# Kernel optimization log

Hardware: AMD Instinct MI355X
Metric: run time of the kernel (lower is better)

## Reference

```python
import jax, jax.numpy as jnp
import numpy as np

B, F, H, LAT = 4, 64, 128, 512
N_CALLS = 16          # n_calls=2, module multiplies by 8
NEG = 0.2             # leaky-relu slope
EPS = 1e-5            # InstanceNorm2d eps

# hypernetwork output layout: w_in[F,3F], b_in[F], w_mid[F,F], b_mid[F], w_out[F,F], b_out[F], w_short[F,3F], b_short[F]
_sizes = [3*F*F, F, F*F, F, F*F, F, 3*F*F, F]
_off = np.cumsum([0] + _sizes)
HYP_OUT = int(_off[-1])


def _sobel_kernel():
    # SinSobel: smoothing (cos) x derivative (sin) separable 5x5 gradient filters
    lin = np.linspace(-1.0, 1.0, 5)
    d = np.sin(lin * np.pi / 2.0)
    s = np.cos(lin * np.pi / 2.0)
    gx = np.outer(s, d)                      # d/dx
    gy = np.outer(d, s)                      # d/dy
    k = np.stack([gx, gy])[:, None]          # [2,1,5,5]
    return jnp.asarray(np.tile(k, (F, 1, 1, 1)), jnp.float32)  # [2F,1,5,5] depthwise


def _conv(x, w, pad, groups=1):
    return jax.lax.conv_general_dilated(
        x, w, (1, 1), [(pad, pad), (pad, pad)],
        dimension_numbers=('NCHW', 'OIHW', 'NCHW'),
        feature_group_count=groups)


def _lrelu(x):
    return jnp.where(x >= 0, x, NEG * x)


def setup_inputs() -> dict:
    key = jax.random.key(0)
    ks = jax.random.split(key, 8)
    f32 = jnp.float32
    return {
        "lat": jax.random.normal(ks[0], (B, LAT), f32),
        "ca_init": jax.random.normal(ks[1], (B, F, H, H), f32),
        "leak_factor": jnp.asarray(0.1, f32),
        "hyper_w": jax.random.normal(ks[2], (HYP_OUT, LAT), f32) * 0.02,
        "hyper_b": jnp.zeros((HYP_OUT,), f32),
        "res_w1": jax.random.normal(ks[3], (F, F, 3, 3), f32) * 0.05,
        "res_b1": jnp.zeros((F,), f32),
        "res_w2": jax.random.normal(ks[4], (F, F, 3, 3), f32) * 0.05,
        "res_b2": jnp.zeros((F,), f32),
        "img_w": jax.random.normal(ks[5], (3, F, 3, 3), f32) * 0.05,
        "img_b": jnp.zeros((3,), f32),
    }


def reference(lat, ca_init, leak_factor, hyper_w, hyper_b,
              res_w1, res_b1, res_w2, res_b2, img_w, img_b):
    sob = _sobel_kernel()
    lf = jnp.clip(leak_factor, 0.001, 1000.0)

    # per-sample dynamic 1x1-conv weights from hypernetwork (lat is loop-invariant)
    ws = lat @ hyper_w.T + hyper_b           # [B, HYP_OUT]

    def seg(i, shape):
        return ws[:, _off[i]:_off[i + 1]].reshape((B,) + shape)
    w_in,  b_in  = seg(0, (F, 3 * F)), seg(1, (F,))
    w_mid, b_mid = seg(2, (F, F)),     seg(3, (F,))
    w_out, b_out = seg(4, (F, F)),     seg(5, (F,))
    w_sh,  b_sh  = seg(6, (F, 3 * F)), seg(7, (F,))

    def step(out, _):
        # SinSobel: identity channels + depthwise 5x5 gradients -> [B,3F,H,H]
        y = jnp.concatenate([out, _conv(out, sob, 2, groups=F)], axis=1)
        # InstanceNorm2d (affine=False)
        mu = y.mean((2, 3), keepdims=True)
        var = y.var((2, 3), keepdims=True)
        y = (y - mu) * jax.lax.rsqrt(var + EPS)
        # DynaResidualBlock: per-sample 1x1 convs (batched GEMMs) + shortcut
        h = _lrelu(jnp.einsum('bchw,boc->bohw', y, w_in) + b_in[:, :, None, None])
        h = _lrelu(jnp.einsum('bchw,boc->bohw', h, w_mid) + b_mid[:, :, None, None])
        h = jnp.einsum('bchw,boc->bohw', h, w_out) + b_out[:, :, None, None]
        sc = jnp.einsum('bchw,boc->bohw', y, w_sh) + b_sh[:, :, None, None]
        return out + lf * (h + sc), None

    out, _ = jax.lax.scan(step, ca_init, None, length=N_CALLS)

    # conv_img: ResidualBlock(3x3) then final 3x3 conv to image channels, clamp
    h = _lrelu(_conv(out, res_w1, 1) + res_b1[None, :, None, None])
    h = _conv(h, res_w2, 1) + res_b2[None, :, None, None]
    out = out + h
    img = _conv(out, img_w, 1) + img_b[None, :, None, None]
    return jnp.clip(img, -1.0, 1.0)
```

## Files before the change

### kernel.cpp

```cpp
#include <hip/hip_runtime.h>
#include <cstddef>

#define R_ 0.70710678118654752f
#define NEG_ 0.2f
#define EPS_ 1e-5f

constexpr int F_ = 64, C3_ = 192, HH_ = 128, NPIX_ = 16384, B_ = 4, LAT_ = 512, HYP_ = 33024;
constexpr int OFFI_WIN = 0, OFFI_BIN = 12288, OFFI_WMID = 12352, OFFI_BMID = 16448,
              OFFI_WOUT = 16512, OFFI_BOUT = 20608, OFFI_WSH = 20672, OFFI_BSH = 32960;
constexpr size_t OFF_HYP = 0;
constexpr size_t OFF_SRAW = 134144;
constexpr size_t OFF_WFIN = 140288;
constexpr size_t OFF_WFSH = 189440;
constexpr size_t OFF_WFMID = 238592;
constexpr size_t OFF_WFOUT = 254976;
constexpr size_t OFF_CW1 = 271360;
constexpr size_t OFF_CW2 = 308224;
constexpr size_t OFF_CWIMG = 345088;
constexpr size_t OFF_OUT = 346816;
constexpr size_t OFF_SOB = 4541120;
constexpr size_t OFF_TMP = OFF_SOB;

typedef short bf16x8 __attribute__((ext_vector_type(8)));
typedef float f32x4 __attribute__((ext_vector_type(4)));

static __device__ __forceinline__ unsigned short f2b(float v) {
  unsigned u = __builtin_bit_cast(unsigned, v);
  u += 0x7fffu + ((u >> 16) & 1u);
  return (unsigned short)(u >> 16);
}
static __device__ __forceinline__ float b2f(unsigned short h) {
  return __builtin_bit_cast(float, ((unsigned)h) << 16);
}
static __device__ __forceinline__ void split2(float v, unsigned short& hi, unsigned short& lo) {
  hi = f2b(v);
  lo = f2b(v - b2f(hi));
}

#define MM3(acc, ahi, alo, whi, wlo)                                        \
  acc = __builtin_amdgcn_mfma_f32_16x16x32_bf16(ahi, whi, acc, 0, 0, 0);    \
  acc = __builtin_amdgcn_mfma_f32_16x16x32_bf16(ahi, wlo, acc, 0, 0, 0);    \
  acc = __builtin_amdgcn_mfma_f32_16x16x32_bf16(alo, whi, acc, 0, 0, 0);

__global__ __launch_bounds__(256) void hyper_gemm_kernel(
    const float* __restrict__ lat, const float* __restrict__ hw,
    const float* __restrict__ hb, float* __restrict__ hyp) {
  __shared__ float slat[B_ * LAT_];
  const int tid = threadIdx.x;
  for (int i = tid; i < B_ * LAT_; i += 256) slat[i] = lat[i];
  __syncthreads();
  const int wave = tid >> 6, lane = tid & 63;
  const int j = blockIdx.x * 4 + wave;
  if (j >= HYP_) return;
  const float* wr = hw + (size_t)j * LAT_;
  float a0 = 0.f, a1 = 0.f, a2 = 0.f, a3 = 0.f;
  for (int i = 0; i < LAT_; i += 64) {
    float w = wr[i + lane];
    a0 = __builtin_fmaf(w, slat[0 * LAT_ + i + lane], a0);
    a1 = __builtin_fmaf(w, slat[1 * LAT_ + i + lane], a1);
    a2 = __builtin_fmaf(w, slat[2 * LAT_ + i + lane], a2);
    a3 = __builtin_fmaf(w, slat[3 * LAT_ + i + lane], a3);
  }
  #pragma unroll
  for (int off = 32; off; off >>= 1) {
    a0 += __shfl_down(a0, off, 64);
    a1 += __shfl_down(a1, off, 64);
    a2 += __shfl_down(a2, off, 64);
    a3 += __shfl_down(a3, off, 64);
  }
  if (lane == 0) {
    float b = hb[j];
    hyp[0 * HYP_ + j] = a0 + b;
    hyp[1 * HYP_ + j] = a1 + b;
    hyp[2 * HYP_ + j] = a2 + b;
    hyp[3 * HYP_ + j] = a3 + b;
  }
}

__global__ __launch_bounds__(256) void prep_dynw_kernel(float* wsm) {
  const int b = blockIdx.x >> 3, sl = blockIdx.x & 7;
  const int tid = threadIdx.x;
  const float* hyp = wsm + OFF_HYP + (size_t)b * HYP_;
  unsigned short* wfin = (unsigned short*)(wsm + OFF_WFIN) + (size_t)b * 24576;
  unsigned short* wfsh = (unsigned short*)(wsm + OFF_WFSH) + (size_t)b * 24576;
  unsigned short* wfmid = (unsigned short*)(wsm + OFF_WFMID) + (size_t)b * 8192;
  unsigned short* wfout = (unsigned short*)(wsm + OFF_WFOUT) + (size_t)b * 8192;

  if (sl < 6) {
    const int base = sl * 2048;
    for (int i = tid; i < 2048; i += 256) {
      int idx = base + i;
      int j = idx & 7, ch = (idx >> 3) & 63, g2 = (idx >> 9) & 3, ks = idx >> 11;
      int k = ks * 32 + g2 * 8 + j;
      int fbx = ((ks * 4 + g2) * 64 + ch) * 16;
      unsigned short h, l;
      split2(hyp[OFFI_WIN + ch * C3_ + k], h, l);
      wfin[fbx + j] = h; wfin[fbx + 8 + j] = l;
      split2(hyp[OFFI_WSH + ch * C3_ + k], h, l);
      wfsh[fbx + j] = h; wfsh[fbx + 8 + j] = l;
    }
  } else if (sl == 6) {
    for (int idx = tid; idx < 4096; idx += 256) {
      int j = idx & 7, ch = (idx >> 3) & 63, g2 = (idx >> 9) & 3, ks = idx >> 11;
      int k = ks * 32 + g2 * 8 + j;
      int fbx = ((ks * 4 + g2) * 64 + ch) * 16;
      unsigned short h, l;
      split2(hyp[OFFI_WMID + ch * 64 + k], h, l);
      wfmid[fbx + j] = h; wfmid[fbx + 8 + j] = l;
      split2(hyp[OFFI_WOUT + ch * 64 + k], h, l);
      wfout[fbx + j] = h; wfout[fbx + 8 + j] = l;
    }
  }
}

__global__ __launch_bounds__(256) void prep_convw_kernel(
    const float* __restrict__ w1, const float* __restrict__ w2,
    const float* __restrict__ wi, unsigned short* __restrict__ wf1,
    unsigned short* __restrict__ wf2, float* __restrict__ wit) {
  const int idx = blockIdx.x * 256 + threadIdx.x;
  if (idx < 36864) {
    int j = idx & 7, ch = (idx >> 3) & 63, fg = idx >> 9;
    int k = (fg >> 2) * 32 + (fg & 3) * 8 + j;
    int c = k & 63, t = k >> 6;
    int fb = (fg * 64 + ch) * 16;
    unsigned short h, l;
    split2(w1[(ch * 64 + c) * 9 + t], h, l);
    wf1[fb + j] = h; wf1[fb + 8 + j] = l;
    split2(w2[(ch * 64 + c) * 9 + t], h, l);
    wf2[fb + j] = h; wf2[fb + 8 + j] = l;
  }
  if (idx < 64 * 9 * 3) {
    int k = idx % 3, rest = idx / 3;
    int t = rest % 9, c = rest / 9;
    wit[idx] = wi[(k * 64 + c) * 9 + t];
  }
}

__device__ __forceinline__ void hline_z(const float* __restrict__ P, int rr, int col,
                                        float& hdv, float& hsv, float& cv) {
  if (rr < 0 || rr > 127) { hdv = 0.f; hsv = 0.f; cv = 0.f; return; }
  const float* rp = P + rr * HH_;
  float vm2 = (col >= 2) ? rp[col - 2] : 0.f;
  float vm1 = (col >= 1) ? rp[col - 1] : 0.f;
  float v0 = rp[col];
  float vp1 = (col <= 126) ? rp[col + 1] : 0.f;
  float vp2 = (col <= 125) ? rp[col + 2] : 0.f;
  hdv = -vm2 - R_ * vm1 + R_ * vp1 + vp2;
  hsv = R_ * vm1 + v0 + R_ * vp1;
  cv = v0;
}

__device__ __forceinline__ float blockReduceSum8(float v, float* scratch) {
  const int tid = threadIdx.x;
  #pragma unroll
  for (int off = 32; off; off >>= 1) v += __shfl_down(v, off, 64);
  if ((tid & 63) == 0) scratch[tid >> 6] = v;
  __syncthreads();
  float r = 0.f;
  #pragma unroll
  for (int w = 0; w < 8; ++w) r += scratch[w];
  __syncthreads();
  return r;
}

__global__ __launch_bounds__(512) void sobel_stats_kernel(
    const float* __restrict__ outb, unsigned int* __restrict__ sob,
    float* __restrict__ sraw) {
  __shared__ float scr[8];
  const int bi = blockIdx.x;
  const int q = bi & 3, c = (bi >> 2) & 63, b = bi >> 8;
  const int tid = threadIdx.x;
  const int col = tid & 127;
  const int r0 = q * 32 + (tid >> 7) * 8;
  const float* P = outb + ((size_t)(b * F_ + c)) * NPIX_;
  unsigned int* ygx = sob + ((size_t)(b * 128 + 2 * c)) * NPIX_;
  unsigned int* ygy = ygx + NPIX_;

  float sI = 0.f, qI = 0.f, sX = 0.f, qX = 0.f, sY = 0.f, qY = 0.f;
  float hd_m1, hd_0, hd_p1, hs_m2, hs_m1, hs_0, hs_p1;
  float td, tc;
  hline_z(P, r0 - 2, col, td, hs_m2, tc);
  hline_z(P, r0 - 1, col, hd_m1, hs_m1, tc);
  hline_z(P, r0, col, hd_0, hs_0, tc);
  sI += tc; qI += tc * tc;
  hline_z(P, r0 + 1, col, hd_p1, hs_p1, tc);
  sI += tc; qI += tc * tc;

  for (int i = 0; i < 8; ++i) {
    const int r = r0 + i;
    const int nr = r + 2;
    float hd_new, hs_new, cnew;
    hline_z(P, nr, col, hd_new, hs_new, cnew);
    if (nr <= r0 + 7) { sI += cnew; qI += cnew * cnew; }
    float gxv = R_ * (hd_m1 + hd_p1) + hd_0;
    float gyv = -hs_m2 - R_ * hs_m1 + R_ * hs_p1 + hs_new;
    const int o = r * HH_ + col;
    unsigned short h, l;
    split2(gxv, h, l);
    ygx[o] = ((unsigned)h << 16) | l;
    split2(gyv, h, l);
    ygy[o] = ((unsigned)h << 16) | l;
    sX += gxv; qX += gxv * gxv;
    sY += gyv; qY += gyv * gyv;
    hd_m1 = hd_0; hd_0 = hd_p1; hd_p1 = hd_new;
    hs_m2 = hs_m1; hs_m1 = hs_0; hs_0 = hs_p1; hs_p1 = hs_new;
  }
  __syncthreads();
  float tI = blockReduceSum8(sI, scr);
  float tQI = blockReduceSum8(qI, scr);
  float tX = blockReduceSum8(sX, scr);
  float tQX = blockReduceSum8(qX, scr);
  float tY = blockReduceSum8(sY, scr);
  float tQY = blockReduceSum8(qY, scr);
  if (tid == 0) {
    float* r = sraw + (size_t)bi * 6;
    r[0] = tI; r[1] = tQI; r[2] = tX; r[3] = tQX; r[4] = tY; r[5] = tQY;
  }
}

__global__ __launch_bounds__(256, 2) void mlp_mfma_kernel(
    float* __restrict__ outb, const unsigned int* __restrict__ sobu,
    const float* __restrict__ wsf, const float* __restrict__ leak) {
  __shared__ unsigned short yhi[64 * 200];
  __shared__ unsigned short ylo[64 * 200];
  __shared__ unsigned short hhi[64 * 72];
  __shared__ unsigned short hlo[64 * 72];
  __shared__ unsigned short resb[64 * 66];
  __shared__ float stl[C3_ * 2];
  __shared__ float ssig[64];
  const int bi = blockIdx.x;
  const int b = bi >> 8, t = bi & 255;
  const int px0 = t * 64;
  const int tid = threadIdx.x;

  if (tid < 64) {
    const int c = tid;
    const float* r = wsf + OFF_SRAW + ((size_t)(b * 64 + c) * 4) * 6;
    float sI = 0.f, qI = 0.f, sX = 0.f, qX = 0.f, sY = 0.f, qY = 0.f;
    #pragma unroll
    for (int q = 0; q < 4; ++q) {
      sI += r[q * 6 + 0]; qI += r[q * 6 + 1];
      sX += r[q * 6 + 2]; qX += r[q * 6 + 3];
      sY += r[q * 6 + 4]; qY += r[q * 6 + 5];
    }
    const float n = 1.f / 16384.f;
    float m, rs;
    m = sI * n; rs = rsqrtf(qI * n - m * m + EPS_);
    stl[c * 2] = m; stl[c * 2 + 1] = rs; ssig[c] = 1.f / rs;
    const int cx = 64 + 2 * c, cy = cx + 1;
    m = sX * n; stl[cx * 2] = m;          stl[cx * 2 + 1] = rsqrtf(qX * n - m * m + EPS_);
    m = sY * n; stl[cy * 2] = m;          stl[cy * 2 + 1] = rsqrtf(qY * n - m * m + EPS_);
  }
  __syncthreads();

  const float* ob = outb + (size_t)b * F_ * NPIX_;
  const unsigned int* sbp = sobu + (size_t)b * 128 * NPIX_;
  #pragma unroll
  for (int it = 0; it < 12; ++it) {
    int ci = it * 256 + tid;
    int k = ci >> 4, pq = ci & 15;
    int kk = k ^ ((pq >> 1) << 3);
    unsigned short* ph = &yhi[(pq * 4) * 200 + kk];
    unsigned short* pl = &ylo[(pq * 4) * 200 + kk];
    const float mu = stl[k * 2], inv = stl[k * 2 + 1];
    float vv[4];
    if (k < 64) {
      float4 f = *(const float4*)(ob + (size_t)k * NPIX_ + px0 + pq * 4);
      vv[0] = f.x; vv[1] = f.y; vv[2] = f.z; vv[3] = f.w;
      const float sg = ssig[k];
      #pragma unroll
      for (int e = 0; e < 4; ++e) {
        unsigned short h, l;
        split2((vv[e] - mu) * inv, h, l);
        ph[e * 200] = h; pl[e * 200] = l;
        float rec = __builtin_fmaf(b2f(h) + b2f(l), sg, mu);
        resb[k * 66 + pq * 4 + e] = f2b(vv[e] - rec);
      }
    } else {
      uint4 v = *(const uint4*)(sbp + (size_t)(k - 64) * NPIX_ + px0 + pq * 4);
      vv[0] = b2f((unsigned short)(v.x >> 16)) + b2f((unsigned short)(v.x & 0xffff));
      vv[1] = b2f((unsigned short)(v.y >> 16)) + b2f((unsigned short)(v.y & 0xffff));
      vv[2] = b2f((unsigned short)(v.z >> 16)) + b2f((unsigned short)(v.z & 0xffff));
      vv[3] = b2f((unsigned short)(v.w >> 16)) + b2f((unsigned short)(v.w & 0xffff));
      #pragma unroll
      for (int e = 0; e < 4; ++e) {
        unsigned short h, l;
        split2((vv[e] - mu) * inv, h, l);
        ph[e * 200] = h; pl[e * 200] = l;
      }
    }
  }
  __syncthreads();

  const int wave = tid >> 6, lane = tid & 63;
  const int lrow = lane & 15, g = lane >> 4;
  const int chm = wave * 16 + lrow;
  const float lf = fminf(fmaxf(leak[0], 0.001f), 1000.f);
  const float* hyp = wsf + OFF_HYP + (size_t)b * HYP_;
  const unsigned short* wfin = (const unsigned short*)(wsf + OFF_WFIN) + (size_t)b * 24576;
  const unsigned short* wfsh = (const unsigned short*)(wsf + OFF_WFSH) + (size_t)b * 24576;
  const unsigned short* wfmid = (const unsigned short*)(wsf + OFF_WFMID) + (size_t)b * 8192;
  const unsigned short* wfout = (const unsigned short*)(wsf + OFF_WFOUT) + (size_t)b * 8192;

  f32x4 aH[4], aS[4];
  {
    float b1 = hyp[OFFI_BIN + chm], b2 = hyp[OFFI_BSH + chm];
    #pragma unroll
    for (int pf = 0; pf < 4; ++pf) {
      aH[pf] = (f32x4){b1, b1, b1, b1};
      aS[pf] = (f32x4){b2, b2, b2, b2};
    }
  }
  #pragma unroll
  for (int ks = 0; ks < 6; ++ks) {
    const size_t wo = (size_t)((ks * 4 + g) * 64 + chm) * 16;
    bf16x8 whiI = *(const bf16x8*)(wfin + wo);
    bf16x8 wloI = *(const bf16x8*)(wfin + wo + 8);
    bf16x8 whiS = *(const bf16x8*)(wfsh + wo);
    bf16x8 wloS = *(const bf16x8*)(wfsh + wo + 8);
    #pragma unroll
    for (int pf = 0; pf < 4; ++pf) {
      const int pxl = pf * 16 + lrow;
      const int kb = pxl * 200 + ((ks * 32 + g * 8) ^ ((pxl >> 3) << 3));
      bf16x8 ahi = *(const bf16x8*)&yhi[kb];
      bf16x8 alo = *(const bf16x8*)&ylo[kb];
      MM3(aH[pf], ahi, alo, whiI, wloI);
      MM3(aS[pf], ahi, alo, whiS, wloS);
    }
  }
  #pragma unroll
  for (int pf = 0; pf < 4; ++pf) {
    #pragma unroll
    for (int j = 0; j < 4; ++j) {
      float v = aH[pf][j];
      v = (v >= 0.f) ? v : NEG_ * v;
      unsigned short h, l;
      split2(v, h, l);
      const int o = (pf * 16 + g * 4 + j) * 72 + chm;
      hhi[o] = h; hlo[o] = l;
    }
  }
  __syncthreads();
  f32x4 aM[4];
  {
    float bm = hyp[OFFI_BMID + chm];
    #pragma unroll
    for (int pf = 0; pf < 4; ++pf) aM[pf] = (f32x4){bm, bm, bm, bm};
  }
  #pragma unroll
  for (int ks = 0; ks < 2; ++ks) {
    const size_t wo = (size_t)((ks * 4 + g) * 64 + chm) * 16;
    bf16x8 whi = *(const bf16x8*)(wfmid + wo);
    bf16x8 wlo = *(const bf16x8*)(wfmid + wo + 8);
    #pragma unroll
    for (int pf = 0; pf < 4; ++pf) {
      const int kb = (pf * 16 + lrow) * 72 + ks * 32 + g * 8;
      bf16x8 ahi = *(const bf16x8*)&hhi[kb];
      bf16x8 alo = *(const bf16x8*)&hlo[kb];
      MM3(aM[pf], ahi, alo, whi, wlo);
    }
  }
  __syncthreads();
  #pragma unroll
  for (int pf = 0; pf < 4; ++pf) {
    #pragma unroll
    for (int j = 0; j < 4; ++j) {
      float v = aM[pf][j];
      v = (v >= 0.f) ? v : NEG_ * v;
      unsigned short h, l;
      split2(v, h, l);
      const int o = (pf * 16 + g * 4 + j) * 72 + chm;
      hhi[o] = h; hlo[o] = l;
    }
  }
  __syncthreads();
  f32x4 aO[4];
  {
    float bo = hyp[OFFI_BOUT + chm];
    #pragma unroll
    for (int pf = 0; pf < 4; ++pf) aO[pf] = (f32x4){bo, bo, bo, bo};
  }
  #pragma unroll
  for (int ks = 0; ks < 2; ++ks) {
    const size_t wo = (size_t)((ks * 4 + g) * 64 + chm) * 16;
    bf16x8 whi = *(const bf16x8*)(wfout + wo);
    bf16x8 wlo = *(const bf16x8*)(wfout + wo + 8);
    #pragma unroll
    for (int pf = 0; pf < 4; ++pf) {
      const int kb = (pf * 16 + lrow) * 72 + ks * 32 + g * 8;
      bf16x8 ahi = *(const bf16x8*)&hhi[kb];
      bf16x8 alo = *(const bf16x8*)&hlo[kb];
      MM3(aO[pf], ahi, alo, whi, wlo);
    }
  }
  const float mu_c = stl[chm * 2];
  const float sg_c = ssig[chm];
  #pragma unroll
  for (int pf = 0; pf < 4; ++pf) {
    float* op = outb + ((size_t)(b * F_ + chm)) * NPIX_ + px0 + pf * 16 + g * 4;
    f32x4 nv;
    #pragma unroll
    for (int j = 0; j < 4; ++j) {
      const int pxl = pf * 16 + g * 4 + j;
      const int kk2 = chm ^ ((pxl >> 3) << 3);
      float yv = b2f(yhi[pxl * 200 + kk2]) + b2f(ylo[pxl * 200 + kk2]);
      float vorig = __builtin_fmaf(yv, sg_c, mu_c) + b2f(resb[chm * 66 + pxl]);
      nv[j] = vorig + lf * (aO[pf][j] + aS[pf][j]);
    }
    *(f32x4*)op = nv;
  }
}

__global__ __launch_bounds__(256, 2) void conv_mfma_kernel(
    const float* __restrict__ in, const unsigned short* __restrict__ wf,
    const float* __restrict__ bias, float* __restrict__ dst, int mode) {
  __shared__ unsigned short ahi[4 * 72 * 64];
  __shared__ unsigned short alo[4 * 72 * 64];
  const int bi = blockIdx.x;
  const int b = bi >> 7, rest = bi & 127;
  const int row0 = (rest >> 1) * 2, colbase = (rest & 1) << 6;
  const int tid = threadIdx.x;
  const float* ip = in + (size_t)b * F_ * NPIX_;

  for (int idx = tid; idx < 4608; idx += 256) {
    const int chunk = idx % 18;
    const int rowp = (idx / 18) % 4;
    const int ch = idx / 72;
    const int r2 = row0 - 1 + rowp;
    const int gcol0 = colbase - 4 + chunk * 4;
    float4 v;
    if (r2 < 0 || r2 > 127) {
      v = make_float4(0.f, 0.f, 0.f, 0.f);
    } else if (gcol0 >= 0 && gcol0 <= 124) {
      v = *(const float4*)(ip + (size_t)ch * NPIX_ + r2 * HH_ + gcol0);
    } else {
      const float* rp = ip + (size_t)ch * NPIX_ + r2 * HH_;
      v.x = (gcol0 >= 0 && gcol0 < 128) ? rp[gcol0] : 0.f;
      v.y = (gcol0 + 1 >= 0 && gcol0 + 1 < 128) ? rp[gcol0 + 1] : 0.f;
      v.z = (gcol0 + 2 >= 0 && gcol0 + 2 < 128) ? rp[gcol0 + 2] : 0.f;
      v.w = (gcol0 + 3 >= 0 && gcol0 + 3 < 128) ? rp[gcol0 + 3] : 0.f;
    }
    const float vv[4] = {v.x, v.y, v.z, v.w};
    #pragma unroll
    for (int e = 0; e < 4; ++e) {
      const int i = chunk * 4 + e;
      const int sw = (((i >> 2) & 7) ^ ((i & 3) << 1) ^ rowp) << 3;
      const int a = (rowp * 72 + i) * 64 + (ch ^ sw);
      unsigned short h, l;
      split2(vv[e], h, l);
      ahi[a] = h; alo[a] = l;
    }
  }
  __syncthreads();

  const int wave = tid >> 6, lane = tid & 63;
  const int lrow = lane & 15, g = lane >> 4;
  const int pxl = wave * 16 + lrow;
  f32x4 acc0[4], acc1[4];
  #pragma unroll
  for (int cg = 0; cg < 4; ++cg) {
    float bz = bias[cg * 16 + lrow];
    acc0[cg] = (f32x4){bz, bz, bz, bz};
    acc1[cg] = (f32x4){bz, bz, bz, bz};
  }
  for (int ks = 0; ks < 18; ++ks) {
    const int kbase = ks * 32 + g * 8;
    const int t = kbase >> 6, c0 = kbase & 63;
    const int dy = t / 3 - 1, dx = t % 3 - 1;
    const int i = pxl + 4 + dx;
    const int rp0 = 1 + dy, rp1 = 2 + dy;
    const int sw0 = (((i >> 2) & 7) ^ ((i & 3) << 1) ^ rp0) << 3;
    const int sw1 = (((i >> 2) & 7) ^ ((i & 3) << 1) ^ rp1) << 3;
    const int a0 = (rp0 * 72 + i) * 64 + (c0 ^ sw0);
    const int a1 = (rp1 * 72 + i) * 64 + (c0 ^ sw1);
    bf16x8 ah0 = *(const bf16x8*)&ahi[a0];
    bf16x8 al0 = *(const bf16x8*)&alo[a0];
    bf16x8 ah1 = *(const bf16x8*)&ahi[a1];
    bf16x8 al1 = *(const bf16x8*)&alo[a1];
    #pragma unroll
    for (int cg = 0; cg < 4; ++cg) {
      const unsigned short* wp = wf + (size_t)((ks * 4 + g) * 64 + cg * 16 + lrow) * 16;
      bf16x8 whi = *(const bf16x8*)wp;
      bf16x8 wlo = *(const bf16x8*)(wp + 8);
      MM3(acc0[cg], ah0, al0, whi, wlo);
      MM3(acc1[cg], ah1, al1, whi, wlo);
    }
  }
  #pragma unroll
  for (int r = 0; r < 2; ++r) {
    #pragma unroll
    for (int cg = 0; cg < 4; ++cg) {
      const f32x4 av = r ? acc1[cg] : acc0[cg];
      float* op = dst + ((size_t)(b * F_ + cg * 16 + lrow)) * NPIX_ + (row0 + r) * HH_ +
                  colbase + wave * 16 + g * 4;
      if (mode == 1) {
        f32x4 rr;
        #pragma unroll
        for (int j = 0; j < 4; ++j) {
          float v = av[j];
          rr[j] = (v >= 0.f) ? v : NEG_ * v;
        }
        *(f32x4*)op = rr;
      } else {
        f32x4 cur = *(f32x4*)op;
        #pragma unroll
        for (int j = 0; j < 4; ++j) cur[j] += av[j];
        *(f32x4*)op = cur;
      }
    }
  }
}

__global__ __launch_bounds__(256, 4) void convimg_kernel(
    const float* __restrict__ outb, const float* __restrict__ wT,
    const float* __restrict__ bias, float* __restrict__ img) {
  __shared__ float part[2 * 128 * 3];
  const int bi = blockIdx.x;
  const int b = bi >> 7, pxb = bi & 127;
  const int tid = threadIdx.x;
  const int px = tid & 127;
  const int hf = __builtin_amdgcn_readfirstlane(tid >> 7);
  const int p = pxb * 128 + px;
  const int row = p >> 7, col = p & 127;
  float a0 = 0.f, a1 = 0.f, a2 = 0.f;
  const float* ip = outb + (size_t)b * F_ * NPIX_;
  for (int cc = 0; cc < 32; ++cc) {
    const int c = hf * 32 + cc;
    const float* pl = ip + (size_t)c * NPIX_;
    #pragma unroll
    for (int t = 0; t < 9; ++t) {
      const int dy = t / 3 - 1, dx = t % 3 - 1;
      const int r2 = row + dy, c2 = col + dx;
      float v = (r2 >= 0 && r2 < 128 && c2 >= 0 && c2 < 128) ? pl[r2 * HH_ + c2] : 0.f;
      const float* wp = wT + (c * 9 + t) * 3;
      a0 = __builtin_fmaf(v, wp[0], a0);
      a1 = __builtin_fmaf(v, wp[1], a1);
      a2 = __builtin_fmaf(v, wp[2], a2);
    }
  }
  part[(hf * 128 + px) * 3 + 0] = a0;
  part[(hf * 128 + px) * 3 + 1] = a1;
  part[(hf * 128 + px) * 3 + 2] = a2;
  __syncthreads();
  if (hf == 0) {
    float r0 = a0 + part[(128 + px) * 3 + 0] + bias[0];
    float r1 = a1 + part[(128 + px) * 3 + 1] + bias[1];
    float r2 = a2 + part[(128 + px) * 3 + 2] + bias[2];
    img[((size_t)b * 3 + 0) * NPIX_ + p] = fminf(fmaxf(r0, -1.f), 1.f);
    img[((size_t)b * 3 + 1) * NPIX_ + p] = fminf(fmaxf(r1, -1.f), 1.f);
    img[((size_t)b * 3 + 2) * NPIX_ + p] = fminf(fmaxf(r2, -1.f), 1.f);
  }
}

extern "C" void kernel_launch(void* const* d_in, const int* in_sizes, int n_in,
                              void* d_out, int out_size, void* d_ws, size_t ws_size,
                              hipStream_t stream) {
  const float* lat = (const float*)d_in[0];
  const float* ca_init = (const float*)d_in[1];
  const float* leak = (const float*)d_in[2];
  const float* hyper_w = (const float*)d_in[3];
  const float* hyper_b = (const float*)d_in[4];
  const float* res_w1 = (const float*)d_in[5];
  const float* res_b1 = (const float*)d_in[6];
  const float* res_w2 = (const float*)d_in[7];
  const float* res_b2 = (const float*)d_in[8];
  const float* img_w = (const float*)d_in[9];
  const float* img_b = (const float*)d_in[10];
  float* out = (float*)d_out;
  float* ws = (float*)d_ws;
  unsigned int* sobu = (unsigned int*)(ws + OFF_SOB);

  hyper_gemm_kernel<<<(HYP_ + 3) / 4, 256, 0, stream>>>(lat, hyper_w, hyper_b, ws + OFF_HYP);
  prep_dynw_kernel<<<32, 256, 0, stream>>>(ws);
  prep_convw_kernel<<<144, 256, 0, stream>>>(res_w1, res_w2, img_w,
                                             (unsigned short*)(ws + OFF_CW1),
                                             (unsigned short*)(ws + OFF_CW2),
                                             ws + OFF_CWIMG);
  hipMemcpyAsync(ws + OFF_OUT, ca_init, (size_t)B_ * F_ * NPIX_ * sizeof(float),
                 hipMemcpyDeviceToDevice, stream);

  for (int st = 0; st < 16; ++st) {
    sobel_stats_kernel<<<1024, 512, 0, stream>>>(ws + OFF_OUT, sobu, ws + OFF_SRAW);
    mlp_mfma_kernel<<<1024, 256, 0, stream>>>(ws + OFF_OUT, sobu, ws, leak);
  }

  conv_mfma_kernel<<<512, 256, 0, stream>>>(ws + OFF_OUT, (const unsigned short*)(ws + OFF_CW1),
                                            res_b1, (float*)(ws + OFF_TMP), 1);
  conv_mfma_kernel<<<512, 256, 0, stream>>>((const float*)(ws + OFF_TMP),
                                            (const unsigned short*)(ws + OFF_CW2),
                                            res_b2, ws + OFF_OUT, 2);
  convimg_kernel<<<512, 256, 0, stream>>>(ws + OFF_OUT, ws + OFF_CWIMG, img_b, out);
}
```

Baseline: 879.8 us.

## Stage MLP input in two channel halves to cut LDS and raise occupancy

The MLP kernel now stages the normalized 192-channel input in two 96-channel chunks, shrinking the shared-memory buffers, and drops the residual side buffer. It re-reads the state from global memory for the final update instead of reconstructing it from LDS. Launch bounds go from 2 to 3 blocks per CU. Separately, the image conv kernel is split into 64-pixel tiles with four channel-quarter waves, doubling the grid. The cost is an extra barrier per MLP block and an additional global read of the state.

New measurement: 852.2 us (median of 2 runs). -3.1%, faster.

```diff
diff --git a/kernel.cpp b/kernel.cpp
--- a/kernel.cpp
+++ b/kernel.cpp
@@ -218,16 +218,14 @@
   }
 }
 
-__global__ __launch_bounds__(256, 2) void mlp_mfma_kernel(
+__global__ __launch_bounds__(256, 3) void mlp_mfma_kernel(
     float* __restrict__ outb, const unsigned int* __restrict__ sobu,
     const float* __restrict__ wsf, const float* __restrict__ leak) {
-  __shared__ unsigned short yhi[64 * 200];
-  __shared__ unsigned short ylo[64 * 200];
-  __shared__ unsigned short hhi[64 * 72];
-  __shared__ unsigned short hlo[64 * 72];
-  __shared__ unsigned short resb[64 * 66];
+  __shared__ unsigned short yhi[64 * 136];
+  __shared__ unsigned short ylo[64 * 136];
+  __shared__ unsigned short hhi[64 * 66];
+  __shared__ unsigned short hlo[64 * 66];
   __shared__ float stl[C3_ * 2];
-  __shared__ float ssig[64];
   const int bi = blockIdx.x;
   const int b = bi >> 8, t = bi & 255;
   const int px0 = t * 64;
@@ -244,9 +242,8 @@
       sY += r[q * 6 + 4]; qY += r[q * 6 + 5];
     }
     const float n = 1.f / 16384.f;
-    float m, rs;
-    m = sI * n; rs = rsqrtf(qI * n - m * m + EPS_);
-    stl[c * 2] = m; stl[c * 2 + 1] = rs; ssig[c] = 1.f / rs;
+    float m;
+    m = sI * n; stl[c * 2] = m;           stl[c * 2 + 1] = rsqrtf(qI * n - m * m + EPS_);
     const int cx = 64 + 2 * c, cy = cx + 1;
     m = sX * n; stl[cx * 2] = m;          stl[cx * 2 + 1] = rsqrtf(qX * n - m * m + EPS_);
     m = sY * n; stl[cy * 2] = m;          stl[cy * 2 + 1] = rsqrtf(qY * n - m * m + EPS_);
@@ -255,43 +252,6 @@
 
   const float* ob = outb + (size_t)b * F_ * NPIX_;
   const unsigned int* sbp = sobu + (size_t)b * 128 * NPIX_;
-  #pragma unroll
-  for (int it = 0; it < 12; ++it) {
-    int ci = it * 256 + tid;
-    int k = ci >> 4, pq = ci & 15;
-    int kk = k ^ ((pq >> 1) << 3);
-    unsigned short* ph = &yhi[(pq * 4) * 200 + kk];
-    unsigned short* pl = &ylo[(pq * 4) * 200 + kk];
-    const float mu = stl[k * 2], inv = stl[k * 2 + 1];
-    float vv[4];
-    if (k < 64) {
-      float4 f = *(const float4*)(ob + (size_t)k * NPIX_ + px0 + pq * 4);
-      vv[0] = f.x; vv[1] = f.y; vv[2] = f.z; vv[3] = f.w;
-      const float sg = ssig[k];
-      #pragma unroll
-      for (int e = 0; e < 4; ++e) {
-        unsigned short h, l;
-        split2((vv[e] - mu) * inv, h, l);
-        ph[e * 200] = h; pl[e * 200] = l;
-        float rec = __builtin_fmaf(b2f(h) + b2f(l), sg, mu);
-        resb[k * 66 + pq * 4 + e] = f2b(vv[e] - rec);
-      }
-    } else {
-      uint4 v = *(const uint4*)(sbp + (size_t)(k - 64) * NPIX_ + px0 + pq * 4);
-      vv[0] = b2f((unsigned short)(v.x >> 16)) + b2f((unsigned short)(v.x & 0xffff));
-      vv[1] = b2f((unsigned short)(v.y >> 16)) + b2f((unsigned short)(v.y & 0xffff));
-      vv[2] = b2f((unsigned short)(v.z >> 16)) + b2f((unsigned short)(v.z & 0xffff));
-      vv[3] = b2f((unsigned short)(v.w >> 16)) + b2f((unsigned short)(v.w & 0xffff));
-      #pragma unroll
-      for (int e = 0; e < 4; ++e) {
-        unsigned short h, l;
-        split2((vv[e] - mu) * inv, h, l);
-        ph[e * 200] = h; pl[e * 200] = l;
-      }
-    }
-  }
-  __syncthreads();
-
   const int wave = tid >> 6, lane = tid & 63;
   const int lrow = lane & 15, g = lane >> 4;
   const int chm = wave * 16 + lrow;
@@ -312,20 +272,56 @@
     }
   }
   #pragma unroll
-  for (int ks = 0; ks < 6; ++ks) {
-    const size_t wo = (size_t)((ks * 4 + g) * 64 + chm) * 16;
-    bf16x8 whiI = *(const bf16x8*)(wfin + wo);
-    bf16x8 wloI = *(const bf16x8*)(wfin + wo + 8);
-    bf16x8 whiS = *(const bf16x8*)(wfsh + wo);
-    bf16x8 wloS = *(const bf16x8*)(wfsh + wo + 8);
-    #pragma unroll
-    for (int pf = 0; pf < 4; ++pf) {
-      const int pxl = pf * 16 + lrow;
-      const int kb = pxl * 200 + ((ks * 32 + g * 8) ^ ((pxl >> 3) << 3));
-      bf16x8 ahi = *(const bf16x8*)&yhi[kb];
-      bf16x8 alo = *(const bf16x8*)&ylo[kb];
-      MM3(aH[pf], ahi, alo, whiI, wloI);
-      MM3(aS[pf], ahi, alo, whiS, wloS);
+  for (int c0 = 0; c0 < 2; ++c0) {
+    if (c0) __syncthreads();
+    #pragma unroll
+    for (int it = 0; it < 6; ++it) {
+      const int ci = it * 256 + tid;
+      const int kl = ci >> 4, pq = ci & 15;
+      const int k = c0 * 96 + kl;
+      const int kk = kl ^ ((pq >> 1) << 3);
+      unsigned short* ph = &yhi[(pq * 4) * 136 + kk];
+      unsigned short* pl = &ylo[(pq * 4) * 136 + kk];
+      const float mu = stl[k * 2], inv = stl[k * 2 + 1];
+      if (k < 64) {
+        float4 f = *(const float4*)(ob + (size_t)k * NPIX_ + px0 + pq * 4);
+        const float vv[4] = {f.x, f.y, f.z, f.w};
+        #pragma unroll
+        for (int e = 0; e < 4; ++e) {
+          unsigned short h, l;
+          split2((vv[e] - mu) * inv, h, l);
+          ph[e * 136] = h; pl[e * 136] = l;
+        }
+      } else {
+        uint4 v = *(const uint4*)(sbp + (size_t)(k - 64) * NPIX_ + px0 + pq * 4);
+        const unsigned uu[4] = {v.x, v.y, v.z, v.w};
+        #pragma unroll
+        for (int e = 0; e < 4; ++e) {
+          float val = b2f((unsigned short)(uu[e] >> 16)) + b2f((unsigned short)(uu[e] & 0xffff));
+          unsigned short h, l;
+          split2((val - mu) * inv, h, l);
+          ph[e * 136] = h; pl[e * 136] = l;
+        }
+      }
+    }
+    __syncthreads();
+    #pragma unroll
+    for (int ks3 = 0; ks3 < 3; ++ks3) {
+      const int ks = c0 * 3 + ks3;
+      const size_t wo = (size_t)((ks * 4 + g) * 64 + chm) * 16;
+      bf16x8 whiI = *(const bf16x8*)(wfin + wo);
+      bf16x8 wloI = *(const bf16x8*)(wfin + wo + 8);
+      bf16x8 whiS = *(const bf16x8*)(wfsh + wo);
+      bf16x8 wloS = *(const bf16x8*)(wfsh + wo + 8);
+      #pragma unroll
+      for (int pf = 0; pf < 4; ++pf) {
+        const int pxl = pf * 16 + lrow;
+        const int kb = pxl * 136 + ((ks3 * 32 + g * 8) ^ ((pxl >> 3) << 3));
+        bf16x8 ahi = *(const bf16x8*)&yhi[kb];
+        bf16x8 alo = *(const bf16x8*)&ylo[kb];
+        MM3(aH[pf], ahi, alo, whiI, wloI);
+        MM3(aS[pf], ahi, alo, whiS, wloS);
+      }
     }
   }
   #pragma unroll
@@ -336,7 +332,7 @@
       v = (v >= 0.f) ? v : NEG_ * v;
       unsigned short h, l;
       split2(v, h, l);
-      const int o = (pf * 16 + g * 4 + j) * 72 + chm;
+      const int o = (pf * 16 + g * 4 + j) * 66 + chm;
       hhi[o] = h; hlo[o] = l;
     }
   }
@@ -354,7 +350,7 @@
     bf16x8 wlo = *(const bf16x8*)(wfmid + wo + 8);
     #pragma unroll
     for (int pf = 0; pf < 4; ++pf) {
-      const int kb = (pf * 16 + lrow) * 72 + ks * 32 + g * 8;
+      const int kb = (pf * 16 + lrow) * 66 + ks * 32 + g * 8;
       bf16x8 ahi = *(const bf16x8*)&hhi[kb];
       bf16x8 alo = *(const bf16x8*)&hlo[kb];
       MM3(aM[pf], ahi, alo, whi, wlo);
@@ -369,7 +365,7 @@
       v = (v >= 0.f) ? v : NEG_ * v;
       unsigned short h, l;
       split2(v, h, l);
-      const int o = (pf * 16 + g * 4 + j) * 72 + chm;
+      const int o = (pf * 16 + g * 4 + j) * 66 + chm;
       hhi[o] = h; hlo[o] = l;
     }
   }
@@ -387,27 +383,19 @@
     bf16x8 wlo = *(const bf16x8*)(wfout + wo + 8);
     #pragma unroll
     for (int pf = 0; pf < 4; ++pf) {
-      const int kb = (pf * 16 + lrow) * 72 + ks * 32 + g * 8;
+      const int kb = (pf * 16 + lrow) * 66 + ks * 32 + g * 8;
       bf16x8 ahi = *(const bf16x8*)&hhi[kb];
       bf16x8 alo = *(const bf16x8*)&hlo[kb];
       MM3(aO[pf], ahi, alo, whi, wlo);
     }
   }
-  const float mu_c = stl[chm * 2];
-  const float sg_c = ssig[chm];
   #pragma unroll
   for (int pf = 0; pf < 4; ++pf) {
     float* op = outb + ((size_t)(b * F_ + chm)) * NPIX_ + px0 + pf * 16 + g * 4;
-    f32x4 nv;
-    #pragma unroll
-    for (int j = 0; j < 4; ++j) {
-      const int pxl = pf * 16 + g * 4 + j;
-      const int kk2 = chm ^ ((pxl >> 3) << 3);
-      float yv = b2f(yhi[pxl * 200 + kk2]) + b2f(ylo[pxl * 200 + kk2]);
-      float vorig = __builtin_fmaf(yv, sg_c, mu_c) + b2f(resb[chm * 66 + pxl]);
-      nv[j] = vorig + lf * (aO[pf][j] + aS[pf][j]);
-    }
-    *(f32x4*)op = nv;
+    f32x4 cur = *(f32x4*)op;
+    #pragma unroll
+    for (int j = 0; j < 4; ++j) cur[j] += lf * (aO[pf][j] + aS[pf][j]);
+    *(f32x4*)op = cur;
   }
 }
 
@@ -514,18 +502,18 @@
 __global__ __launch_bounds__(256, 4) void convimg_kernel(
     const float* __restrict__ outb, const float* __restrict__ wT,
     const float* __restrict__ bias, float* __restrict__ img) {
-  __shared__ float part[2 * 128 * 3];
+  __shared__ float part[4 * 64 * 3];
   const int bi = blockIdx.x;
-  const int b = bi >> 7, pxb = bi & 127;
-  const int tid = threadIdx.x;
-  const int px = tid & 127;
-  const int hf = __builtin_amdgcn_readfirstlane(tid >> 7);
-  const int p = pxb * 128 + px;
+  const int b = bi >> 8, tile = bi & 255;
+  const int tid = threadIdx.x;
+  const int px = tid & 63;
+  const int hf = __builtin_amdgcn_readfirstlane(tid >> 6);
+  const int p = tile * 64 + px;
   const int row = p >> 7, col = p & 127;
   float a0 = 0.f, a1 = 0.f, a2 = 0.f;
   const float* ip = outb + (size_t)b * F_ * NPIX_;
-  for (int cc = 0; cc < 32; ++cc) {
-    const int c = hf * 32 + cc;
+  for (int cc = 0; cc < 16; ++cc) {
+    const int c = hf * 16 + cc;
     const float* pl = ip + (size_t)c * NPIX_;
     #pragma unroll
     for (int t = 0; t < 9; ++t) {
@@ -538,14 +526,18 @@
       a2 = __builtin_fmaf(v, wp[2], a2);
     }
   }
-  part[(hf * 128 + px) * 3 + 0] = a0;
-  part[(hf * 128 + px) * 3 + 1] = a1;
-  part[(hf * 128 + px) * 3 + 2] = a2;
+  part[(hf * 64 + px) * 3 + 0] = a0;
+  part[(hf * 64 + px) * 3 + 1] = a1;
+  part[(hf * 64 + px) * 3 + 2] = a2;
   __syncthreads();
   if (hf == 0) {
-    float r0 = a0 + part[(128 + px) * 3 + 0] + bias[0];
-    float r1 = a1 + part[(128 + px) * 3 + 1] + bias[1];
-    float r2 = a2 + part[(128 + px) * 3 + 2] + bias[2];
+    float r0 = a0 + bias[0], r1 = a1 + bias[1], r2 = a2 + bias[2];
+    #pragma unroll
+    for (int w = 1; w < 4; ++w) {
+      r0 += part[(w * 64 + px) * 3 + 0];
+      r1 += part[(w * 64 + px) * 3 + 1];
+      r2 += part[(w * 64 + px) * 3 + 2];
+    }
     img[((size_t)b * 3 + 0) * NPIX_ + p] = fminf(fmaxf(r0, -1.f), 1.f);
     img[((size_t)b * 3 + 1) * NPIX_ + p] = fminf(fmaxf(r1, -1.f), 1.f);
     img[((size_t)b * 3 + 2) * NPIX_ + p] = fminf(fmaxf(r2, -1.f), 1.f);
@@ -589,5 +581,5 @@
   conv_mfma_kernel<<<512, 256, 0, stream>>>((const float*)(ws + OFF_TMP),
                                             (const unsigned short*)(ws + OFF_CW2),
                                             res_b2, ws + OFF_OUT, 2);
-  convimg_kernel<<<512, 256, 0, stream>>>(ws + OFF_OUT, ws + OFF_CWIMG, img_b, out);
-}
+  convimg_kernel<<<1024, 256, 0, stream>>>(ws + OFF_OUT, ws + OFF_CWIMG, img_b, out);
+}
```
